# Kernel optimization log

Hardware: AMD Instinct MI355X
Metric: run time of the kernel (lower is better)

The kernel has to match this reference:

```python
import jax, jax.numpy as jnp
import numpy as np

C_IN = 34   # C*V = 2*17 channels after reshape
C_MID = 16
C_OUT = 3
N_LAYERS = 3
BN_EPS = 1e-5
NEG_SLOPE = 0.01


def setup_inputs() -> dict:
    key = jax.random.key(0)
    ks = jax.random.split(key, 16)
    B, C, T, V = 512, 2, 2048, 17
    s = 1.0 / np.sqrt(C_IN)
    inp = {
        "x": jax.random.normal(ks[0], (B, C, T, V), dtype=jnp.float32),
        # stacked per-layer 1x1-conv (linear) weights for Q/K/V of 3 attention layers
        "wq": jax.random.normal(ks[1], (N_LAYERS, C_IN, C_IN), dtype=jnp.float32) * s,
        "bq": jax.random.normal(ks[2], (N_LAYERS, C_IN), dtype=jnp.float32) * 0.02,
        "wk": jax.random.normal(ks[3], (N_LAYERS, C_IN, C_IN), dtype=jnp.float32) * s,
        "bk": jax.random.normal(ks[4], (N_LAYERS, C_IN), dtype=jnp.float32) * 0.02,
        "wv": jax.random.normal(ks[5], (N_LAYERS, C_IN, C_IN), dtype=jnp.float32) * s,
        "bv": jax.random.normal(ks[6], (N_LAYERS, C_IN), dtype=jnp.float32) * 0.02,
        # head: conv1 -> BN -> LeakyReLU -> conv2
        "w1": jax.random.normal(ks[7], (C_MID, C_IN), dtype=jnp.float32) * s,
        "b1": jax.random.normal(ks[8], (C_MID,), dtype=jnp.float32) * 0.02,
        "gamma": jnp.ones((C_MID,), dtype=jnp.float32),
        "beta": jnp.zeros((C_MID,), dtype=jnp.float32),
        "mean": jax.random.normal(ks[9], (C_MID,), dtype=jnp.float32) * 0.1,
        "var": jax.random.uniform(ks[10], (C_MID,), dtype=jnp.float32, minval=0.5, maxval=1.5),
        "w2": jax.random.normal(ks[11], (C_OUT, C_MID), dtype=jnp.float32) * (1.0 / np.sqrt(C_MID)),
        "b2": jax.random.normal(ks[12], (C_OUT,), dtype=jnp.float32) * 0.02,
    }
    return inp


def _conv1x1(w, b, h):
    # 1x1 Conv1d == linear over channel dim: (O,C) x (B,C,T) -> (B,O,T)
    return jnp.einsum('oc,bct->bot', w, h) + b[:, None]


def reference(x, wq, bq, wk, bk, wv, bv, w1, b1, gamma, beta, mean, var, w2, b2):
    B, C, T, V = x.shape
    h = x.transpose(0, 1, 3, 2).reshape(B, C * V, T)  # (B, 34, T)
    scale = 1.0 / (T ** 0.5)  # K.size(-1) ** 0.5 in the original
    for i in range(N_LAYERS):
        Q = _conv1x1(wq[i], bq[i], h)
        K = _conv1x1(wk[i], bk[i], h)
        Vv = _conv1x1(wv[i], bv[i], h)
        scores = jnp.einsum('bct,bdt->bcd', Q, K) * scale  # (B, 34, 34) channel attention
        attn = jax.nn.softmax(scores, axis=-1)
        h = jnp.einsum('bcd,bdt->bct', attn, Vv)
    y = _conv1x1(w1, b1, h)                               # (B, 16, T)
    inv = gamma / jnp.sqrt(var + BN_EPS)                  # inference-mode BatchNorm1d
    y = (y - mean[:, None]) * inv[:, None] + beta[:, None]
    y = jnp.where(y > 0, y, NEG_SLOPE * y)                # LeakyReLU
    return _conv1x1(w2, b2, y)                            # (B, 3, T)
```

## Files before the change

kernel.cpp:

```cpp
#include <hip/hip_runtime.h>

#define CV   34
#define TTOT 2048
#define NB   512
#define XB   69632
#define XC   34816

#define RB_STRIDE 576

typedef __attribute__((ext_vector_type(8))) short v8s;
typedef __attribute__((ext_vector_type(4))) float v4f;

__device__ __forceinline__ unsigned short f2bf(float f) {
    unsigned int u = __float_as_uint(f);
    u = u + 0x7FFFu + ((u >> 16) & 1u);
    return (unsigned short)(u >> 16);
}
__device__ __forceinline__ float bf2f(unsigned short s) {
    return __uint_as_float(((unsigned int)s) << 16);
}

__device__ __forceinline__ unsigned int cvtpk_bf16(float a, float b) {
    unsigned int r;
    asm("v_cvt_pk_bf16_f32 %0, %1, %2" : "=v"(r) : "v"(a), "v"(b));
    return r;
}

__device__ __forceinline__ void split8(const float (&f)[8], v8s* hi, v8s* lo) {
    union { unsigned int u[4]; v8s s; } H, L;
#pragma unroll
    for (int p = 0; p < 4; ++p) {
        float a = f[2 * p], b = f[2 * p + 1];
        unsigned int h = cvtpk_bf16(a, b);
        float ra = a - __uint_as_float(h << 16);
        float rb = b - __uint_as_float(h & 0xFFFF0000u);
        L.u[p] = cvtpk_bf16(ra, rb);
        H.u[p] = h;
    }
    *hi = H.s;
    *lo = L.s;
}

__device__ __forceinline__ void stage_chunk(const float* __restrict__ xb, int t0,
                                            float* rawbuf, int w, int lane) {
#pragma unroll
    for (int i = 0; i < 5; ++i) {
        int idx = i * 4 + w;
        if (idx < 17) {
            int fl = idx * 256 + lane * 4;
            int co = (fl >= 2176) ? 1 : 0;
            const float* g = xb + t0 * 17 + fl + co * 32640;
            __builtin_amdgcn_global_load_lds(
                (const __attribute__((address_space(1))) void*)g,
                (__attribute__((address_space(3))) void*)(rawbuf + idx * 256),
                16, 0, 0);
        }
    }
}

#define RST 44
#define RSZ (36 * RST)
#define R_G0 0
#define R_At (1 * RSZ)
#define R_Aq (2 * RSZ)
#define R_Ak (3 * RSZ)
#define R_Av (4 * RSZ)
#define R_S1 (5 * RSZ)
#define R_Sc (6 * RSZ)
#define R_Wx (7 * RSZ)
#define SMF  (8 * RSZ)
#define STF  17408

__device__ __forceinline__ void ldfrag8(const float* p, v8s* hi, v8s* lo) {
    float f[8];
    *(float4*)&f[0] = *(const float4*)p;
    *(float4*)&f[4] = *(const float4*)(p + 4);
    split8(f, hi, lo);
}

__device__ __forceinline__ void ldfrag4(const float* p, int quad, v8s* hi, v8s* lo) {
    union { unsigned int u[4]; v8s s; } H, L;
#pragma unroll
    for (int i = 0; i < 4; ++i) { H.u[i] = 0; L.u[i] = 0; }
    if (quad == 0) {
        float4 f = *(const float4*)p;
        unsigned int h0 = cvtpk_bf16(f.x, f.y);
        unsigned int h1 = cvtpk_bf16(f.z, f.w);
        float r0 = f.x - __uint_as_float(h0 << 16);
        float r1 = f.y - __uint_as_float(h0 & 0xFFFF0000u);
        float r2 = f.z - __uint_as_float(h1 << 16);
        float r3 = f.w - __uint_as_float(h1 & 0xFFFF0000u);
        H.u[0] = h0; H.u[1] = h1;
        L.u[0] = cvtpk_bf16(r0, r1);
        L.u[1] = cvtpk_bf16(r2, r3);
    }
    *hi = H.s;
    *lo = L.s;
}

__device__ __forceinline__ void tile_mm(float* __restrict__ SMD, int Lo, int Ro,
                                        int Do, int tm, int tn, int lane,
                                        bool transD) {
    const int lc = lane & 15, quad = lane >> 4;
    int ra = tm * 16 + lc; ra = ra < 36 ? ra : 35;
    const float* pa = SMD + Lo + ra * RST;
    v8s Ah0, Al0, Ah1, Al1;
    ldfrag8(pa + quad * 8, &Ah0, &Al0);
    ldfrag4(pa + 32, quad, &Ah1, &Al1);
    int rb = tn * 16 + lc; rb = rb < 36 ? rb : 35;
    const float* pb = SMD + Ro + rb * RST;
    v8s Bh0, Bl0, Bh1, Bl1;
    ldfrag8(pb + quad * 8, &Bh0, &Bl0);
    ldfrag4(pb + 32, quad, &Bh1, &Bl1);
    v4f acc = {0.f, 0.f, 0.f, 0.f};
    acc = __builtin_amdgcn_mfma_f32_16x16x32_bf16(Ah0, Bh0, acc, 0, 0, 0);
    acc = __builtin_amdgcn_mfma_f32_16x16x32_bf16(Ah0, Bl0, acc, 0, 0, 0);
    acc = __builtin_amdgcn_mfma_f32_16x16x32_bf16(Al0, Bh0, acc, 0, 0, 0);
    acc = __builtin_amdgcn_mfma_f32_16x16x32_bf16(Ah1, Bh1, acc, 0, 0, 0);
    acc = __builtin_amdgcn_mfma_f32_16x16x32_bf16(Ah1, Bl1, acc, 0, 0, 0);
    acc = __builtin_amdgcn_mfma_f32_16x16x32_bf16(Al1, Bh1, acc, 0, 0, 0);
    if (!transD) {
        int gcol = tn * 16 + lc;
        if (gcol < 36) {
#pragma unroll
            for (int i = 0; i < 4; ++i) {
                int grow = tm * 16 + quad * 4 + i;
                if (grow < 36) SMD[Do + grow * RST + gcol] = acc[i];
            }
        }
    } else {
        int trow = tn * 16 + lc;
        int tcol = tm * 16 + quad * 4;
        if (trow < 36 && tcol < 36)
            *(v4f*)&SMD[Do + trow * RST + tcol] = acc;
    }
}

__global__ __launch_bounds__(512) void k_fused(
    const float* __restrict__ x,
    const float* __restrict__ wq, const float* __restrict__ bq,
    const float* __restrict__ wk, const float* __restrict__ bk,
    const float* __restrict__ wv, const float* __restrict__ bv,
    const float* __restrict__ w1, const float* __restrict__ b1,
    const float* __restrict__ gamma, const float* __restrict__ beta,
    const float* __restrict__ mean, const float* __restrict__ var,
    float* __restrict__ ws) {
    __shared__ __align__(16) float SMD[STF];
    const int tid  = threadIdx.x;
    const int wave = tid >> 6;
    const int wsub = wave & 3;
    const int g    = wave >> 2;
    const int l    = tid & 63;
    const int b    = blockIdx.x;
    const int row16 = l & 15;
    const int quad  = l >> 4;
    const float* xb = x + (size_t)b * XB;

    int offc[3];
#pragma unroll
    for (int r = 0; r < 3; ++r) {
        int c = r * 16 + row16;
        if (c > 33) c = 33;
        offc[r] = (c >= 17) ? (2159 + c) : c;
    }
    const int koff = wsub * 32 + quad * 8;

    v4f accG[3][3];
    v4f accS[3];
    {
        v4f vz = {0.f, 0.f, 0.f, 0.f};
#pragma unroll
        for (int r = 0; r < 3; ++r) {
            accS[r] = vz;
#pragma unroll
            for (int c = 0; c < 3; ++c) accG[r][c] = vz;
        }
    }
    v8s ones;
#pragma unroll
    for (int i = 0; i < 8; ++i) ones[i] = (short)0x3F80;

    float* buf0 = SMD + (g * 2 + 0) * 4352;
    float* buf1 = SMD + (g * 2 + 1) * 4352;

    stage_chunk(xb, g * 128, buf0, wsub, l);
    __syncthreads();

    for (int i = 0; i < 8; ++i) {
        const int myChunk = 2 * i + g;
        float* cur = (i & 1) ? buf1 : buf0;
        float* nxt = (i & 1) ? buf0 : buf1;
        if (i < 7) stage_chunk(xb, (myChunk + 2) * 128, nxt, wsub, l);

        const float* rb = cur + koff * 17;
        v8s fh[3], fl4[3];
#pragma unroll
        for (int r = 0; r < 3; ++r) {
            const float* p = rb + offc[r];
            float f[8];
#pragma unroll
            for (int e = 0; e < 8; ++e) f[e] = p[e * 17];
            split8(f, &fh[r], &fl4[r]);
        }
#pragma unroll
        for (int r = 0; r < 3; ++r) {
#pragma unroll
            for (int c = 0; c < 3; ++c) {
                accG[r][c] = __builtin_amdgcn_mfma_f32_16x16x32_bf16(fh[r],  fh[c],  accG[r][c], 0, 0, 0);
                accG[r][c] = __builtin_amdgcn_mfma_f32_16x16x32_bf16(fh[r],  fl4[c], accG[r][c], 0, 0, 0);
                accG[r][c] = __builtin_amdgcn_mfma_f32_16x16x32_bf16(fl4[r], fh[c],  accG[r][c], 0, 0, 0);
            }
            accS[r] = __builtin_amdgcn_mfma_f32_16x16x32_bf16(fh[r],  ones, accS[r], 0, 0, 0);
            accS[r] = __builtin_amdgcn_mfma_f32_16x16x32_bf16(fl4[r], ones, accS[r], 0, 0, 0);
        }
        __syncthreads();
    }

    {
        float* gp = SMD + wave * RSZ;
#pragma unroll
        for (int r = 0; r < 3; ++r) {
#pragma unroll
            for (int c = 0; c < 3; ++c) {
#pragma unroll
                for (int i = 0; i < 4; ++i) {
                    int m = r * 16 + quad * 4 + i;
                    int n = c * 16 + row16;
                    if (m < 34 && n < 34) gp[m * RST + n] = accG[r][c][i];
                }
            }
            if (row16 == 0) {
#pragma unroll
                for (int i = 0; i < 4; ++i) {
                    int m = r * 16 + quad * 4 + i;
                    if (m < 34) gp[34 * RST + m] = accS[r][i];
                }
            }
        }
    }
    __syncthreads();
    float gred[3];
    int   gm[3], gn[3];
#pragma unroll
    for (int k = 0; k < 3; ++k) {
        int idx = tid + k * 512;
        if (idx < 1156) {
            int m = idx / 34, n = idx - m * 34;
            gm[k] = m; gn[k] = n;
            float s = 0.f;
#pragma unroll
            for (int r = 0; r < 8; ++r) s += SMD[r * RSZ + m * RST + n];
            gred[k] = s;
        } else { gm[k] = -1; gn[k] = 0; gred[k] = 0.f; }
    }
    float s0red = 0.f;
    if (tid < 34) {
#pragma unroll
        for (int r = 0; r < 8; ++r) s0red += SMD[r * RSZ + 34 * RST + tid];
    }
    __syncthreads();
    {
        const float4 z = make_float4(0.f, 0.f, 0.f, 0.f);
        for (int i = tid * 4; i < SMF; i += 2048) *(float4*)(SMD + i) = z;
    }
    __syncthreads();
#pragma unroll
    for (int k = 0; k < 3; ++k)
        if (gm[k] >= 0) SMD[R_G0 + gm[k] * RST + gn[k]] = gred[k];
    for (int idx = tid; idx < 1156; idx += 512) {
        int m = idx / 34, n = idx - m * 34;
        SMD[R_Aq + m * RST + n] = wq[idx];
        SMD[R_Ak + m * RST + n] = wk[idx];
        SMD[R_Av + n * RST + m] = wv[idx];
    }
    if (tid < 34) {
        SMD[R_G0 + 34 * RST + tid] = s0red;
        SMD[R_G0 + tid * RST + 34] = s0red;
        SMD[R_Aq + tid * RST + 34] = bq[tid];
        SMD[R_Ak + tid * RST + 34] = bk[tid];
        SMD[R_Av + 34 * RST + tid] = bv[tid];
    }
    if (tid == 0) SMD[R_G0 + 34 * RST + 34] = 2048.0f;
    __syncthreads();

    for (int lyr = 0; lyr < 3; ++lyr) {
        if (lyr > 0) {
            const float* wql = wq + lyr * 1156;
            const float* wkl = wk + lyr * 1156;
            const float* wvl = wv + lyr * 1156;
            for (int idx = tid; idx < 1156; idx += 512) {
                int m = idx / 34, n = idx - m * 34;
                SMD[R_S1 + m * RST + n] = wql[idx];
                SMD[R_Sc + m * RST + n] = wkl[idx];
                SMD[R_Wx + m * RST + n] = wvl[idx];
            }
            __syncthreads();
            for (int t = wave; t < 27; t += 8) {
                int mmI = t / 9, tile = t - mmI * 9;
                int tm = tile / 3, tn = tile - tm * 3;
                int Lo = (mmI == 0) ? R_S1 : (mmI == 1) ? R_Sc : R_Wx;
                int Do = (mmI == 0) ? R_Aq : (mmI == 1) ? R_Ak : R_Av;
                tile_mm(SMD, Lo, R_At, Do, tm, tn, l, mmI == 2);
            }
            __syncthreads();
            if (tid < 34) {
                SMD[R_Aq + tid * RST + 34] += bq[lyr * 34 + tid];
                SMD[R_Ak + tid * RST + 34] += bk[lyr * 34 + tid];
                SMD[R_Av + 34 * RST + tid] += bv[lyr * 34 + tid];
            }
            __syncthreads();
        }
        for (int t = wave; t < 9; t += 8) {
            int tm = t / 3, tn = t - tm * 3;
            tile_mm(SMD, R_Aq, R_G0, R_S1, tm, tn, l, false);
        }
        __syncthreads();
        for (int t = wave; t < 9; t += 8) {
            int tm = t / 3, tn = t - tm * 3;
            tile_mm(SMD, R_S1, R_Ak, R_Sc, tm, tn, l, false);
        }
        __syncthreads();
        if (tid < 34) {
            float f[36];
#pragma unroll
            for (int e0 = 0; e0 < 36; e0 += 4)
                *(float4*)&f[e0] = *(const float4*)&SMD[R_Sc + tid * RST + e0];
            const float scale = 0.022097086912079608f;
            float mx = -1e30f;
#pragma unroll
            for (int d = 0; d < 34; ++d) { f[d] *= scale; mx = fmaxf(mx, f[d]); }
            float sum = 0.f;
#pragma unroll
            for (int d = 0; d < 34; ++d) { float e = __expf(f[d] - mx); f[d] = e; sum += e; }
            float rs = 1.0f / sum;
#pragma unroll
            for (int d = 0; d < 34; ++d) f[d] *= rs;
            f[34] = 0.f; f[35] = 0.f;
#pragma unroll
            for (int e0 = 0; e0 < 36; e0 += 4)
                *(float4*)&SMD[R_Sc + tid * RST + e0] = *(const float4*)&f[e0];
        } else if (tid >= 64 && tid < 82) {
            int u = tid - 64;
            int row = 34 + u / 9, c4 = (u - (u / 9) * 9) * 4;
            *(float4*)&SMD[R_Sc + row * RST + c4] = make_float4(0.f, 0.f, 0.f, 0.f);
        }
        __syncthreads();
        for (int t = wave; t < 9; t += 8) {
            int tm = t / 3, tn = t - tm * 3;
            tile_mm(SMD, R_Av, R_Sc, R_At, tm, tn, l, false);
        }
        __syncthreads();
    }

    for (int idx = tid; idx < 544; idx += 512) {
        int m = idx / 34, n = idx - m * 34;
        SMD[R_Sc + m * RST + n] = w1[idx];
    }
    __syncthreads();
    for (int t = wave; t < 9; t += 8) {
        int tm = t / 3, tn = t - tm * 3;
        tile_mm(SMD, R_Sc, R_At, R_S1, tm, tn, l, false);
    }
    __syncthreads();
    float* wb = ws + (size_t)b * RB_STRIDE;
    if (tid < 16) {
        float iv = gamma[tid] * rsqrtf(var[tid] + 1e-5f);
        float cyraw = SMD[R_S1 + tid * RST + 34] + b1[tid];
        wb[512 + tid] = (cyraw - mean[tid]) * iv + beta[tid];
        wb[528 + tid] = SMD[R_S1 + tid * RST + 32] * iv;
        wb[544 + tid] = SMD[R_S1 + tid * RST + 33] * iv;
    }
    unsigned short* wp = (unsigned short*)wb;
    for (int i = tid; i < 512; i += 512) {
        int o = i >> 5, c = i & 31;
        float iv = gamma[o] * rsqrtf(var[o] + 1e-5f);
        float vv = SMD[R_S1 + o * RST + c] * iv;
        unsigned short hb = f2bf(vv);
        wp[i] = hb;
        wp[512 + i] = f2bf(vv - bf2f(hb));
    }
}

__global__ __launch_bounds__(256, 4) void k_out(const float* __restrict__ x,
                                                const float* __restrict__ w2,
                                                const float* __restrict__ b2,
                                                const float* __restrict__ ws,
                                                float* __restrict__ out) {
    __shared__ __align__(16) float raw[2][4352];

    const int tid  = threadIdx.x;
    const int b    = blockIdx.x >> 3;
    const int seg  = (blockIdx.x & 7) * 256;
    const int l    = tid & 63;
    const int w    = tid >> 6;
    const int quad = l >> 4;
    const int col  = l & 15;

    const float* wb = ws + (size_t)b * RB_STRIDE;
    const unsigned short* wp = (const unsigned short*)wb;
    v8s aH = *(const v8s*)&wp[col * 32 + quad * 8];
    v8s aL = *(const v8s*)&wp[512 + col * 32 + quad * 8];
    float cyr[4], w2r[3][4], wy32r[4], wy33r[4];
#pragma unroll
    for (int i = 0; i < 4; ++i) {
        int o = quad * 4 + i;
        cyr[i]   = wb[512 + o];
        wy32r[i] = wb[528 + o];
        wy33r[i] = wb[544 + o];
#pragma unroll
        for (int p = 0; p < 3; ++p) w2r[p][i] = w2[p * 16 + o];
    }
    float b2r[3] = {b2[0], b2[1], b2[2]};
    const float* xb = x + (size_t)b * XB;

    int offq[8];
#pragma unroll
    for (int e = 0; e < 8; ++e) {
        int c = quad * 8 + e;
        offq[e] = (c >= 17) ? (2159 + c) : c;
    }

    stage_chunk(xb, seg, raw[0], w, l);
    __syncthreads();

    for (int ch = 0; ch < 2; ++ch) {
        if (ch == 0) stage_chunk(xb, seg + 128, raw[1], w, l);
        for (int tt = w; tt < 8; tt += 4) {
            const int tl = tt * 16 + col;
            const float* rbt = raw[ch] + tl * 17;
            float f[8];
#pragma unroll
            for (int e = 0; e < 8; ++e) f[e] = rbt[offq[e]];
            v8s bH, bL;
            split8(f, &bH, &bL);
            v4f acc = {0.f, 0.f, 0.f, 0.f};
            acc = __builtin_amdgcn_mfma_f32_16x16x32_bf16(aH, bH, acc, 0, 0, 0);
            acc = __builtin_amdgcn_mfma_f32_16x16x32_bf16(aH, bL, acc, 0, 0, 0);
            acc = __builtin_amdgcn_mfma_f32_16x16x32_bf16(aL, bH, acc, 0, 0, 0);
            float h32 = rbt[2191];
            float h33 = rbt[2192];
            float op[3] = {0, 0, 0};
#pragma unroll
            for (int i = 0; i < 4; ++i) {
                float y = acc[i] + cyr[i] + wy32r[i] * h32 + wy33r[i] * h33;
                float z = (y > 0.f) ? y : 0.01f * y;
#pragma unroll
                for (int p = 0; p < 3; ++p) op[p] += w2r[p][i] * z;
            }
#pragma unroll
            for (int p = 0; p < 3; ++p) {
                op[p] += __shfl_xor(op[p], 16);
                op[p] += __shfl_xor(op[p], 32);
            }
            if (l < 16) {
                int tg = seg + ch * 128 + tt * 16 + l;
#pragma unroll
                for (int p = 0; p < 3; ++p)
                    out[((size_t)b * 3 + p) * 2048 + tg] = op[p] + b2r[p];
            }
        }
        __syncthreads();
    }
}

extern "C" void kernel_launch(void* const* d_in, const int* in_sizes, int n_in,
                              void* d_out, int out_size, void* d_ws, size_t ws_size,
                              hipStream_t stream) {
    const float* x     = (const float*)d_in[0];
    const float* wq    = (const float*)d_in[1];
    const float* bq    = (const float*)d_in[2];
    const float* wk    = (const float*)d_in[3];
    const float* bk    = (const float*)d_in[4];
    const float* wv    = (const float*)d_in[5];
    const float* bv    = (const float*)d_in[6];
    const float* w1    = (const float*)d_in[7];
    const float* b1    = (const float*)d_in[8];
    const float* gamma = (const float*)d_in[9];
    const float* beta  = (const float*)d_in[10];
    const float* mean  = (const float*)d_in[11];
    const float* var   = (const float*)d_in[12];
    const float* w2    = (const float*)d_in[13];
    const float* b2    = (const float*)d_in[14];
    float* ws  = (float*)d_ws;
    float* out = (float*)d_out;

    k_fused<<<dim3(512), dim3(512), 0, stream>>>(x, wq, bq, wk, bk, wv, bv,
                                                 w1, b1, gamma, beta, mean, var, ws);
    k_out<<<dim3(4096), dim3(256), 0, stream>>>(x, w2, b2, ws, out);
}
```

Before: 278.6 us.

## Fuse output head kernel into attention kernel, dropping workspace round-trip

Folds the k_out output stage into k_fused so each batch's 512-thread block computes its folded head weights in shared memory, then streams all 16 time chunks of x itself. Two wave groups each handle alternate chunks with double-buffered staging. This removes the second launch and the workspace write and read. In exchange there are only 512 blocks instead of 4096 for the bandwidth-bound output pass, and the fused kernel's shared-memory footprint limits occupancy, so memory parallelism may fall.

```diff
diff --git a/kernel.cpp b/kernel.cpp
--- a/kernel.cpp
+++ b/kernel.cpp
@@ -5,8 +5,6 @@
 #define NB   512
 #define XB   69632
 #define XC   34816
-
-#define RB_STRIDE 576
 
 typedef __attribute__((ext_vector_type(8))) short v8s;
 typedef __attribute__((ext_vector_type(4))) float v4f;
@@ -144,7 +142,8 @@
     const float* __restrict__ w1, const float* __restrict__ b1,
     const float* __restrict__ gamma, const float* __restrict__ beta,
     const float* __restrict__ mean, const float* __restrict__ var,
-    float* __restrict__ ws) {
+    const float* __restrict__ w2, const float* __restrict__ b2,
+    float* __restrict__ out) {
     __shared__ __align__(16) float SMD[STF];
     const int tid  = threadIdx.x;
     const int wave = tid >> 6;
@@ -362,56 +361,30 @@
         tile_mm(SMD, R_Sc, R_At, R_S1, tm, tn, l, false);
     }
     __syncthreads();
-    float* wb = ws + (size_t)b * RB_STRIDE;
-    if (tid < 16) {
-        float iv = gamma[tid] * rsqrtf(var[tid] + 1e-5f);
-        float cyraw = SMD[R_S1 + tid * RST + 34] + b1[tid];
-        wb[512 + tid] = (cyraw - mean[tid]) * iv + beta[tid];
-        wb[528 + tid] = SMD[R_S1 + tid * RST + 32] * iv;
-        wb[544 + tid] = SMD[R_S1 + tid * RST + 33] * iv;
-    }
-    unsigned short* wp = (unsigned short*)wb;
-    for (int i = tid; i < 512; i += 512) {
-        int o = i >> 5, c = i & 31;
-        float iv = gamma[o] * rsqrtf(var[o] + 1e-5f);
-        float vv = SMD[R_S1 + o * RST + c] * iv;
-        unsigned short hb = f2bf(vv);
-        wp[i] = hb;
-        wp[512 + i] = f2bf(vv - bf2f(hb));
-    }
-}
-
-__global__ __launch_bounds__(256, 4) void k_out(const float* __restrict__ x,
-                                                const float* __restrict__ w2,
-                                                const float* __restrict__ b2,
-                                                const float* __restrict__ ws,
-                                                float* __restrict__ out) {
-    __shared__ __align__(16) float raw[2][4352];
-
-    const int tid  = threadIdx.x;
-    const int b    = blockIdx.x >> 3;
-    const int seg  = (blockIdx.x & 7) * 256;
-    const int l    = tid & 63;
-    const int w    = tid >> 6;
-    const int quad = l >> 4;
-    const int col  = l & 15;
-
-    const float* wb = ws + (size_t)b * RB_STRIDE;
-    const unsigned short* wp = (const unsigned short*)wb;
-    v8s aH = *(const v8s*)&wp[col * 32 + quad * 8];
-    v8s aL = *(const v8s*)&wp[512 + col * 32 + quad * 8];
+
+    const int col = l & 15;
+    v8s aH, aL;
+    {
+        float iv_o = gamma[col] * rsqrtf(var[col] + 1e-5f);
+        float fv[8];
+#pragma unroll
+        for (int j = 0; j < 8; ++j)
+            fv[j] = SMD[R_S1 + col * RST + quad * 8 + j] * iv_o;
+        split8(fv, &aH, &aL);
+    }
     float cyr[4], w2r[3][4], wy32r[4], wy33r[4];
 #pragma unroll
     for (int i = 0; i < 4; ++i) {
         int o = quad * 4 + i;
-        cyr[i]   = wb[512 + o];
-        wy32r[i] = wb[528 + o];
-        wy33r[i] = wb[544 + o];
+        float iv = gamma[o] * rsqrtf(var[o] + 1e-5f);
+        cyr[i]   = (SMD[R_S1 + o * RST + 34] + b1[o] - mean[o]) * iv + beta[o];
+        wy32r[i] = SMD[R_S1 + o * RST + 32] * iv;
+        wy33r[i] = SMD[R_S1 + o * RST + 33] * iv;
 #pragma unroll
         for (int p = 0; p < 3; ++p) w2r[p][i] = w2[p * 16 + o];
     }
     float b2r[3] = {b2[0], b2[1], b2[2]};
-    const float* xb = x + (size_t)b * XB;
+    __syncthreads();
 
     int offq[8];
 #pragma unroll
@@ -420,14 +393,18 @@
         offq[e] = (c >= 17) ? (2159 + c) : c;
     }
 
-    stage_chunk(xb, seg, raw[0], w, l);
-    __syncthreads();
-
-    for (int ch = 0; ch < 2; ++ch) {
-        if (ch == 0) stage_chunk(xb, seg + 128, raw[1], w, l);
-        for (int tt = w; tt < 8; tt += 4) {
+    stage_chunk(xb, g * 128, buf0, wsub, l);
+    __syncthreads();
+
+    for (int i = 0; i < 8; ++i) {
+        const int myChunk = 2 * i + g;
+        float* cur = (i & 1) ? buf1 : buf0;
+        float* nxt = (i & 1) ? buf0 : buf1;
+        if (i < 7) stage_chunk(xb, (myChunk + 2) * 128, nxt, wsub, l);
+
+        for (int tt = wsub; tt < 8; tt += 4) {
             const int tl = tt * 16 + col;
-            const float* rbt = raw[ch] + tl * 17;
+            const float* rbt = cur + tl * 17;
             float f[8];
 #pragma unroll
             for (int e = 0; e < 8; ++e) f[e] = rbt[offq[e]];
@@ -441,11 +418,11 @@
             float h33 = rbt[2192];
             float op[3] = {0, 0, 0};
 #pragma unroll
-            for (int i = 0; i < 4; ++i) {
-                float y = acc[i] + cyr[i] + wy32r[i] * h32 + wy33r[i] * h33;
+            for (int i2 = 0; i2 < 4; ++i2) {
+                float y = acc[i2] + cyr[i2] + wy32r[i2] * h32 + wy33r[i2] * h33;
                 float z = (y > 0.f) ? y : 0.01f * y;
 #pragma unroll
-                for (int p = 0; p < 3; ++p) op[p] += w2r[p][i] * z;
+                for (int p = 0; p < 3; ++p) op[p] += w2r[p][i2] * z;
             }
 #pragma unroll
             for (int p = 0; p < 3; ++p) {
@@ -453,7 +430,7 @@
                 op[p] += __shfl_xor(op[p], 32);
             }
             if (l < 16) {
-                int tg = seg + ch * 128 + tt * 16 + l;
+                int tg = myChunk * 128 + tt * 16 + l;
 #pragma unroll
                 for (int p = 0; p < 3; ++p)
                     out[((size_t)b * 3 + p) * 2048 + tg] = op[p] + b2r[p];
@@ -481,10 +458,9 @@
     const float* var   = (const float*)d_in[12];
     const float* w2    = (const float*)d_in[13];
     const float* b2    = (const float*)d_in[14];
-    float* ws  = (float*)d_ws;
     float* out = (float*)d_out;
 
     k_fused<<<dim3(512), dim3(512), 0, stream>>>(x, wq, bq, wk, bk, wv, bv,
-                                                 w1, b1, gamma, beta, mean, var, ws);
-    k_out<<<dim3(4096), dim3(256), 0, stream>>>(x, w2, b2, ws, out);
-}
+                                                 w1, b1, gamma, beta, mean, var,
+                                                 w2, b2, out);
+}
```

Measured after the change: 289.8 us. +4.0%, slower.
